# Optimization experiments

Hardware: AMD Instinct MI355X
Metric: run time of the kernel (lower is better)

The kernel has to match this reference:

```python
import jax, jax.numpy as jnp
import numpy as np

KSIZE = 3  # kernel_size from init_kwargs


def _unfold_same(x, ks):
    """Torch nn.Unfold with fixed 'same' padding. x:(B,C,H,W) -> (B, C*ks*ks, H, W).
    Channel ordering matches torch unfold: (c, kh, kw) with c outermost."""
    B, C, H, W = x.shape
    pad_total = ks - 1
    pb = pad_total // 2
    pe = pad_total - pb
    xp = jnp.pad(x, ((0, 0), (0, 0), (pb, pe), (pb, pe)))
    # small fixed loop over ks*ks = 9 taps
    patches = jnp.stack(
        [xp[:, :, di:di + H, dj:dj + W] for di in range(ks) for dj in range(ks)],
        axis=2,
    )  # (B, C, ks*ks, H, W)
    return patches.reshape(B, C * ks * ks, H, W)


def setup_inputs() -> dict:
    key = jax.random.key(0)
    k1, k2 = jax.random.split(key)
    B, C, H, W = 16, 32, 256, 256
    O, ks = 64, KSIZE
    K = C * ks * ks  # 288
    x = jax.random.normal(k1, (B, C, H, W), dtype=jnp.float32)
    limit = float(np.sqrt(6.0 / (K + O)))  # xavier_uniform
    weight = jax.random.uniform(k2, (O, K), jnp.float32, -limit, limit)
    bias = jnp.zeros((O, 1), dtype=jnp.float32)
    return {"x": x, "weight": weight, "bias": bias}


def reference(x, weight, bias):
    # Faithful math of Linear.forward: same-padded unfold, then per-pixel
    # out[n,o] = sum_k weight[o,k] * patch[n,k] + bias[o], reshaped to (B,O,H,W).
    # Expressed as a single contraction instead of the (N,O,K) broadcast intermediate.
    patches = _unfold_same(x, KSIZE)                     # (B, K, H, W)
    out = jnp.einsum('ok,bkhw->bohw', weight, patches)   # (B, O, H, W)
    out = out + bias.reshape(1, -1, 1, 1)
    return out
```

## Files before the change

### kernel.cpp

```cpp
#include <hip/hip_runtime.h>
#include <hip/hip_bf16.h>

#define CIN 32
#define OCH 64
#define HH  256
#define WW  256
#define HW  (HH * WW)
#define BH  8
#define ROWB (258 * 64)

typedef __bf16 bf16x8 __attribute__((ext_vector_type(8)));
typedef float  f32x4  __attribute__((ext_vector_type(4)));
typedef float  f32x16 __attribute__((ext_vector_type(16)));

__global__ __launch_bounds__(256, 1) void conv_fused_kernel(
        const float* __restrict__ x, const float* __restrict__ wgt,
        const float* __restrict__ bias, float* __restrict__ out) {
    const int bid = blockIdx.x;
    const int nid = (bid & 7) * 64 + (bid >> 3);
    const int b   = nid >> 5;
    const int h0  = (nid & 31) * BH;
    const int tid = threadIdx.x;
    const int l   = tid & 63, wid = tid >> 6;
    const int lw  = l & 31,  hi  = l >> 5;
    const int og  = wid & 1;
    const int wf  = wid >> 1;

    __shared__ __bf16 xs[4][258][CIN];
    char* lds = (char*)&xs[0][0][0];
    const float* xb = x + (size_t)b * CIN * HW;

    if (tid < 32) {
        const int s = tid >> 3, k = tid & 7;
        const int wp = (k < 4) ? 0 : 257;
        *(f32x4*)(lds + s * ROWB + wp * 64 + (k & 3) * 16) = (f32x4){0, 0, 0, 0};
    }

    bf16x8 af[9][2];
    {
        const float* wrow = wgt + (size_t)(og * 32 + lw) * 288 + hi * 72;
#pragma unroll
        for (int ks = 0; ks < 2; ++ks)
#pragma unroll
            for (int t = 0; t < 9; ++t)
#pragma unroll
                for (int j = 0; j < 8; ++j)
                    af[t][ks][j] = (__bf16)wrow[ks * 144 + j * 9 + t];
    }
    const float bsc = bias[og * 32 + lw];

    auto stage = [&](int row) {
        char* slot = lds + ((row + 1) & 3) * ROWB;
        if (row >= 0 && row < HH) {
            const float* rp = xb + (size_t)row * WW;
            f32x4 v[8];
#pragma unroll
            for (int j = 0; j < 8; ++j)
                v[j] = *(const f32x4*)(rp + (size_t)(wid * 8 + j) * HW + 4 * l);
#pragma unroll
            for (int p = 0; p < 4; ++p) {
                const int w = 4 * l + p;
                bf16x8 pk;
#pragma unroll
                for (int j = 0; j < 8; ++j) pk[j] = (__bf16)v[j][p];
                *(bf16x8*)(slot + (w + 1) * 64 + ((wid ^ ((w >> 1) & 3)) << 4)) = pk;
            }
        } else {
#pragma unroll
            for (int p = 0; p < 4; ++p) {
                const int w = 4 * l + p;
                *(f32x4*)(slot + (w + 1) * 64 + ((wid ^ ((w >> 1) & 3)) << 4)) =
                    (f32x4){0, 0, 0, 0};
            }
        }
    };

    stage(h0 - 1); stage(h0); stage(h0 + 1);

    int off6[3][2];
#pragma unroll
    for (int kw = 0; kw < 3; ++kw) {
        const int e = lw + kw;
        const int m = (e == 0) ? 3 : (((e - 1) >> 1) & 3);
#pragma unroll
        for (int ks = 0; ks < 2; ++ks)
            off6[kw][ks] = e * 64 + (((ks * 2 + hi) ^ m) << 4);
    }
    const int halfoff = wf * (128 * 64);

    __syncthreads();

    for (int i = 0; i < BH; ++i) {
        const int h  = h0 + i;
        const int nr = h + 2;
        const bool havenext = (i < BH - 1);
        const bool rok2 = havenext && (nr < HH);

        f32x4 v[8];
#pragma unroll
        for (int j = 0; j < 8; ++j) v[j] = (f32x4){0, 0, 0, 0};
        if (rok2) {
            const float* rp = xb + (size_t)nr * WW;
#pragma unroll
            for (int j = 0; j < 8; ++j)
                v[j] = *(const f32x4*)(rp + (size_t)(wid * 8 + j) * HW + 4 * l);
        }

        const char* s0 = lds + ((h    ) & 3) * ROWB + halfoff;
        const char* s1 = lds + ((h + 1) & 3) * ROWB + halfoff;
        const char* s2 = lds + ((h + 2) & 3) * ROWB + halfoff;
        f32x16 acc[4];
#pragma unroll
        for (int t = 0; t < 4; ++t)
#pragma unroll
            for (int r = 0; r < 16; ++r) acc[t][r] = bsc;
#pragma unroll
        for (int t = 0; t < 4; ++t) {
#pragma unroll
            for (int kh = 0; kh < 3; ++kh) {
                const char* s = (kh == 0) ? s0 : (kh == 1) ? s1 : s2;
#pragma unroll
                for (int ks = 0; ks < 2; ++ks)
#pragma unroll
                    for (int kw = 0; kw < 3; ++kw) {
                        bf16x8 bf = *(const bf16x8*)(s + t * 2048 + off6[kw][ks]);
                        acc[t] = __builtin_amdgcn_mfma_f32_32x32x16_bf16(
                            bf, af[kh * 3 + kw][ks], acc[t], 0, 0, 0);
                    }
            }
        }

        float* outb = out + ((size_t)b * OCH + og * 32 + lw) * HW +
                      (size_t)h * WW + wf * 128 + 4 * hi;
#pragma unroll
        for (int t = 0; t < 4; ++t)
#pragma unroll
            for (int q = 0; q < 4; ++q) {
                f32x4 val = { acc[t][4 * q], acc[t][4 * q + 1],
                              acc[t][4 * q + 2], acc[t][4 * q + 3] };
                *(f32x4*)(outb + t * 32 + 8 * q) = val;
            }

        if (havenext) {
            char* slot = lds + ((nr + 1) & 3) * ROWB;
#pragma unroll
            for (int p = 0; p < 4; ++p) {
                const int w = 4 * l + p;
                bf16x8 pk;
#pragma unroll
                for (int j = 0; j < 8; ++j) pk[j] = (__bf16)v[j][p];
                *(bf16x8*)(slot + (w + 1) * 64 + ((wid ^ ((w >> 1) & 3)) << 4)) = pk;
            }
            __builtin_amdgcn_sched_barrier(0);
            asm volatile("s_waitcnt lgkmcnt(0)" ::: "memory");
            __builtin_amdgcn_s_barrier();
            __builtin_amdgcn_sched_barrier(0);
        }
    }
}

extern "C" void kernel_launch(void* const* d_in, const int* in_sizes, int n_in,
                              void* d_out, int out_size, void* d_ws, size_t ws_size,
                              hipStream_t stream) {
    const float* x    = (const float*)d_in[0];
    const float* w    = (const float*)d_in[1];
    const float* bias = (const float*)d_in[2];
    float* out = (float*)d_out;

    hipLaunchKernelGGL(conv_fused_kernel, dim3(512), dim3(256), 0, stream,
                       x, w, bias, out);
}
```

Measured before the change: 110.7 us.

## Pre-convert input to swizzled bf16 NHWC and stream rows via global_load_lds

Adds a prep kernel that converts the fp32 NCHW input into a bf16 channel-last, pre-swizzled layout in workspace. The main conv kernel then streams each row straight into LDS with async global_load_lds instead of loading fp32 into registers, converting, and writing to LDS. This removes the in-loop conversion and register staging and halves the bytes read per row inside the conv, but adds a second launch plus an extra full write and read of the bf16 copy. The original fused kernel remains as a fallback when the workspace is too small.

After: 125.3 us. +13.2%, slower.

```diff
diff --git a/kernel.cpp b/kernel.cpp
--- a/kernel.cpp
+++ b/kernel.cpp
@@ -8,12 +8,189 @@
 #define HW  (HH * WW)
 #define BH  8
 #define ROWB (258 * 64)
+#define XROWB (WW * CIN * 2)
 
 typedef __bf16 bf16x8 __attribute__((ext_vector_type(8)));
 typedef float  f32x4  __attribute__((ext_vector_type(4)));
 typedef float  f32x16 __attribute__((ext_vector_type(16)));
 
-__global__ __launch_bounds__(256, 1) void conv_fused_kernel(
+typedef __attribute__((address_space(3))) unsigned int lds_u32;
+typedef const __attribute__((address_space(1))) unsigned int glb_u32;
+
+__device__ inline void gload_lds16(const void* g, void* l) {
+    __builtin_amdgcn_global_load_lds((glb_u32*)g, (lds_u32*)l, 16, 0, 0);
+}
+
+__global__ __launch_bounds__(256) void xprep_kernel(const float* __restrict__ x,
+                                                    __bf16* __restrict__ xt) {
+    const int h = blockIdx.x, b = blockIdx.y;
+    const int tid = threadIdx.x;
+    const int cg = tid >> 6;
+    const int wl = tid & 63;
+
+    __shared__ __bf16 ls[WW][CIN];
+
+    const float* xb = x + ((size_t)b * CIN + cg * 8) * HW + (size_t)h * WW;
+#pragma unroll
+    for (int wh = 0; wh < 2; ++wh) {
+        const int w0 = wh * 128 + wl * 2;
+        float2 v[8];
+#pragma unroll
+        for (int j = 0; j < 8; ++j)
+            v[j] = *(const float2*)(xb + (size_t)j * HW + w0);
+#pragma unroll
+        for (int p = 0; p < 2; ++p) {
+            const int w = w0 + p;
+            bf16x8 pk;
+#pragma unroll
+            for (int j = 0; j < 8; ++j) pk[j] = (__bf16)(p ? v[j].y : v[j].x);
+            const int sp = cg ^ ((w >> 1) & 3);
+            *(bf16x8*)((char*)&ls[0][0] + w * 64 + sp * 16) = pk;
+        }
+    }
+    __syncthreads();
+
+    f32x4* dst = (f32x4*)((char*)xt + ((size_t)b * HH + h) * XROWB);
+    const f32x4* src = (const f32x4*)&ls[0][0];
+#pragma unroll
+    for (int q = 0; q < 4; ++q)
+        dst[q * 256 + tid] = src[q * 256 + tid];
+}
+
+__global__ __launch_bounds__(256, 1) void conv_main_kernel(
+        const __bf16* __restrict__ xt, const float* __restrict__ wgt,
+        const float* __restrict__ bias, float* __restrict__ out) {
+    const int bid = blockIdx.x;
+    const int nid = (bid & 7) * 64 + (bid >> 3);
+    const int b   = nid >> 5;
+    const int h0  = (nid & 31) * BH;
+    const int tid = threadIdx.x;
+    const int l   = tid & 63, wid = tid >> 6;
+    const int lw  = l & 31,  hi  = l >> 5;
+    const int og  = wid & 1;
+    const int wf  = wid >> 1;
+
+    __shared__ char lds4[4][ROWB];
+    char* lds = &lds4[0][0];
+    const char* xtb = (const char*)xt + (size_t)b * HH * XROWB;
+
+    if (tid < 32) {
+        const int s = tid >> 3, k = tid & 7;
+        const int wp = (k < 4) ? 0 : 257;
+        *(f32x4*)(lds + s * ROWB + wp * 64 + (k & 3) * 16) = (f32x4){0, 0, 0, 0};
+    }
+
+    bf16x8 af[9][2];
+    {
+        const float* wrow = wgt + (size_t)(og * 32 + lw) * 288 + hi * 72;
+#pragma unroll
+        for (int ks = 0; ks < 2; ++ks)
+#pragma unroll
+            for (int t = 0; t < 9; ++t)
+#pragma unroll
+                for (int j = 0; j < 8; ++j)
+                    af[t][ks][j] = (__bf16)wrow[ks * 144 + j * 9 + t];
+    }
+    const float bsc = bias[og * 32 + lw];
+
+#pragma unroll
+    for (int r = 0; r < 3; ++r) {
+        const int row = h0 - 1 + r;
+        char* slot = lds + ((row + 1) & 3) * ROWB + 64;
+        if (row >= 0) {
+            const char* src = xtb + (size_t)row * XROWB;
+#pragma unroll
+            for (int k = 0; k < 4; ++k) {
+                const int o4 = (wid * 4 + k) * 1024 + l * 16;
+                gload_lds16(src + o4, slot + o4);
+            }
+        } else {
+#pragma unroll
+            for (int k = 0; k < 4; ++k)
+                *(f32x4*)(slot + (wid * 4 + k) * 1024 + l * 16) = (f32x4){0, 0, 0, 0};
+        }
+    }
+
+    int off6[3][2];
+#pragma unroll
+    for (int kw = 0; kw < 3; ++kw) {
+        const int e = lw + kw;
+        const int m = (e == 0) ? 3 : (((e - 1) >> 1) & 3);
+#pragma unroll
+        for (int ks = 0; ks < 2; ++ks)
+            off6[kw][ks] = e * 64 + (((ks * 2 + hi) ^ m) << 4);
+    }
+    const int halfoff = wf * (128 * 64);
+
+    __syncthreads();
+
+    for (int i = 0; i < BH; ++i) {
+        const int h = h0 + i;
+
+        if (i < BH - 1) {
+            const int rs = h + 2;
+            char* slot = lds + ((rs + 1) & 3) * ROWB + 64;
+            if (rs < HH) {
+                const char* src = xtb + (size_t)rs * XROWB;
+#pragma unroll
+                for (int k = 0; k < 4; ++k) {
+                    const int o4 = (wid * 4 + k) * 1024 + l * 16;
+                    gload_lds16(src + o4, slot + o4);
+                }
+            } else {
+#pragma unroll
+                for (int k = 0; k < 4; ++k)
+                    *(f32x4*)(slot + (wid * 4 + k) * 1024 + l * 16) =
+                        (f32x4){0, 0, 0, 0};
+            }
+        }
+        __builtin_amdgcn_sched_barrier(0);
+
+        const char* s0 = lds + ((h    ) & 3) * ROWB + halfoff;
+        const char* s1 = lds + ((h + 1) & 3) * ROWB + halfoff;
+        const char* s2 = lds + ((h + 2) & 3) * ROWB + halfoff;
+        f32x16 acc[4];
+#pragma unroll
+        for (int t = 0; t < 4; ++t)
+#pragma unroll
+            for (int r = 0; r < 16; ++r) acc[t][r] = bsc;
+#pragma unroll
+        for (int t = 0; t < 4; ++t) {
+#pragma unroll
+            for (int kh = 0; kh < 3; ++kh) {
+                const char* s = (kh == 0) ? s0 : (kh == 1) ? s1 : s2;
+#pragma unroll
+                for (int ks = 0; ks < 2; ++ks)
+#pragma unroll
+                    for (int kw = 0; kw < 3; ++kw) {
+                        bf16x8 bf = *(const bf16x8*)(s + t * 2048 + off6[kw][ks]);
+                        acc[t] = __builtin_amdgcn_mfma_f32_32x32x16_bf16(
+                            bf, af[kh * 3 + kw][ks], acc[t], 0, 0, 0);
+                    }
+            }
+        }
+
+        float* outb = out + ((size_t)b * OCH + og * 32 + lw) * HW +
+                      (size_t)h * WW + wf * 128 + 4 * hi;
+#pragma unroll
+        for (int t = 0; t < 4; ++t)
+#pragma unroll
+            for (int q = 0; q < 4; ++q) {
+                f32x4 val = { acc[t][4 * q], acc[t][4 * q + 1],
+                              acc[t][4 * q + 2], acc[t][4 * q + 3] };
+                *(f32x4*)(outb + t * 32 + 8 * q) = val;
+            }
+
+        if (i < BH - 1) {
+            __builtin_amdgcn_sched_barrier(0);
+            asm volatile("s_waitcnt vmcnt(16) lgkmcnt(0)" ::: "memory");
+            __builtin_amdgcn_s_barrier();
+            __builtin_amdgcn_sched_barrier(0);
+        }
+    }
+}
+
+__global__ __launch_bounds__(256, 1) void conv_fallback_kernel(
         const float* __restrict__ x, const float* __restrict__ wgt,
         const float* __restrict__ bias, float* __restrict__ out) {
     const int bid = blockIdx.x;
@@ -35,7 +212,6 @@
         const int wp = (k < 4) ? 0 : 257;
         *(f32x4*)(lds + s * ROWB + wp * 64 + (k & 3) * 16) = (f32x4){0, 0, 0, 0};
     }
-
     bf16x8 af[9][2];
     {
         const float* wrow = wgt + (size_t)(og * 32 + lw) * 288 + hi * 72;
@@ -74,7 +250,6 @@
             }
         }
     };
-
     stage(h0 - 1); stage(h0); stage(h0 + 1);
 
     int off6[3][2];
@@ -167,6 +342,14 @@
     const float* bias = (const float*)d_in[2];
     float* out = (float*)d_out;
 
-    hipLaunchKernelGGL(conv_fused_kernel, dim3(512), dim3(256), 0, stream,
-                       x, w, bias, out);
-}
+    const size_t XT_BYTES = (size_t)16 * HH * XROWB;
+    if (ws_size >= XT_BYTES) {
+        __bf16* xt = (__bf16*)d_ws;
+        hipLaunchKernelGGL(xprep_kernel, dim3(HH, 16), dim3(256), 0, stream, x, xt);
+        hipLaunchKernelGGL(conv_main_kernel, dim3(512), dim3(256), 0, stream,
+                           xt, w, bias, out);
+    } else {
+        hipLaunchKernelGGL(conv_fallback_kernel, dim3(512), dim3(256), 0, stream,
+                           x, w, bias, out);
+    }
+}
```
